# Performance work log

Hardware: AMD Instinct MI355X
Metric: run time of the kernel (lower is better)

The kernel has to match this reference:

```python
import jax, jax.numpy as jnp
import numpy as np

N, P = 65536, 1024

def setup_inputs() -> dict:
    key = jax.random.key(0)
    k1, k2, k3, k4 = jax.random.split(key, 4)
    X = jax.random.normal(k1, (N, P), dtype=jnp.float32)
    beta0 = jax.random.normal(k2, (1,), dtype=jnp.float32)
    beta = jax.random.normal(k3, (P,), dtype=jnp.float32)
    Theta = jax.random.normal(k4, (P, P), dtype=jnp.float32)
    return {"X": X, "beta0": beta0, "beta": beta, "Theta": Theta}

def reference(X, beta0, beta, Theta):
    # y_hat = beta0 + X @ beta + sum_{j<k} Theta[j,k] * X[:,j] * X[:,k]
    # The double loop uses only the strictly upper-triangular part of Theta.
    p = Theta.shape[0]
    theta_upper = jnp.triu(Theta, k=1)                     # [p, p]
    linear = beta0 + X @ beta                              # [n]
    interaction = jnp.sum((X @ theta_upper) * X, axis=1)   # [n], quadratic form
    return linear + interaction
```

## Files before the change

kernel.cpp:

```cpp
#include <hip/hip_runtime.h>


typedef __bf16 bf16_t;
typedef bf16_t bf16x8 __attribute__((ext_vector_type(8)));
typedef float f32x4 __attribute__((ext_vector_type(4)));
typedef unsigned short u16;
typedef u16 u16x4 __attribute__((ext_vector_type(4)));
typedef u16 u16x8 __attribute__((ext_vector_type(8)));

#define N_ROWS 65536
#define P_DIM  1024
#define BM 128
#define BN 128
#define BK 64

static __device__ __forceinline__ u16 f2bf(float f) {
  unsigned u = __builtin_bit_cast(unsigned, f);
  u += 0x7FFFu + ((u >> 16) & 1u);
  return (u16)(u >> 16);
}
static __device__ __forceinline__ float bf2f(u16 v) {
  return __builtin_bit_cast(float, ((unsigned)v) << 16);
}

static __device__ __forceinline__ void gload16(const void* g, void* lds_base) {
  __builtin_amdgcn_global_load_lds(
      (const __attribute__((address_space(1))) unsigned char*)g,
      (__attribute__((address_space(3))) unsigned char*)lds_base, 16, 0, 0);
}

__global__ void __launch_bounds__(256)
init_y(float* __restrict__ y, const float* __restrict__ beta0) {
  int i = blockIdx.x * blockDim.x + threadIdx.x;
  if (i < N_ROWS) y[i] = beta0[0];
}

__global__ void __launch_bounds__(256)
conv_x(const float* __restrict__ X, u16* __restrict__ Xb,
       float* __restrict__ y, const float* __restrict__ beta0) {
  const size_t tg = (size_t)blockIdx.x * 256 + threadIdx.x;
  if (tg < N_ROWS) y[tg] = beta0[0];
  const size_t nq = (size_t)N_ROWS * P_DIM / 8;
  const size_t stride = (size_t)gridDim.x * 256;
  for (size_t i = tg; i < nq; i += stride) {
    const int row = (int)(i >> 7);
    const int q   = (int)(i & 127);
    f32x4 a = *(const f32x4*)(X + i * 8);
    f32x4 b = *(const f32x4*)(X + i * 8 + 4);
    u16x8 w;
    #pragma unroll
    for (int j = 0; j < 4; ++j) { w[j] = f2bf(a[j]); w[j + 4] = f2bf(b[j]); }
    *(u16x8*)(Xb + (size_t)row * P_DIM + (size_t)((q ^ (row & 7)) * 8)) = w;
  }
}

__global__ void __launch_bounds__(128)
conv_theta(const float* __restrict__ Theta, u16* __restrict__ Tt) {
  __shared__ float tile[32][33];
  const int tid = threadIdx.x;
  const int k0  = blockIdx.x * 32;
  const int c0  = blockIdx.y * 32;
  {
    const int tx = tid & 31;
    const int rb = tid >> 5;
    #pragma unroll
    for (int i = 0; i < 8; ++i) {
      int kl = rb * 8 + i;
      tile[kl][tx] = Theta[(size_t)(k0 + kl) * P_DIM + c0 + tx];
    }
  }
  __syncthreads();
  {
    const int cl = tid >> 2;
    const int qt = tid & 3;
    const int c  = c0 + cl;
    const int Q  = blockIdx.x * 4 + qt;
    u16x8 w;
    #pragma unroll
    for (int e = 0; e < 8; ++e) {
      int k = Q * 8 + e;
      float v = tile[qt * 8 + e][cl];
      w[e] = (k < c) ? f2bf(v) : (u16)0;
    }
    *(u16x8*)(Tt + (size_t)c * P_DIM + (size_t)((Q ^ (c & 7)) * 8)) = w;
  }
}

__global__ void __launch_bounds__(512)
gemm_r12(const u16* __restrict__ Xb, const u16* __restrict__ Tt,
         const float* __restrict__ beta, float* __restrict__ y)
{
  __shared__ __align__(16) u16 L[2][16384];

  const int nwg = (N_ROWS / BM) * (P_DIM / BN);
  const int swz = (blockIdx.x & 7) * (nwg / 8) + (blockIdx.x >> 3);
  const int bn  = 7 - (swz & 7);
  const int bm  = swz >> 3;
  const int c0  = bn * BN;
  const int m0  = bm * BM;
  const int nkt = (bn + 1) * 2;

  const int tid  = threadIdx.x;
  const int lane = tid & 63;
  const int wid  = tid >> 6;
  const int wm   = wid >> 1;
  const int wn   = wid & 1;
  const int l15  = lane & 15;
  const int lg   = lane >> 4;

  const int srow = lane >> 3;
  const int sq   = (lane & 7) * 8;

  f32x4 acc[2][4];
  #pragma unroll
  for (int i = 0; i < 2; ++i)
    #pragma unroll
    for (int j = 0; j < 4; ++j)
      acc[i][j] = (f32x4)0.0f;

  #define STAGE(buf_, t_)                                                       \
    {                                                                           \
      const int kk_ = (t_) * BK;                                                \
      _Pragma("unroll")                                                         \
      for (int q = 0; q < 2; ++q) {                                             \
        const int ch_ = wid * 2 + q;                                            \
        gload16(Xb + (size_t)(m0 + ch_ * 8 + srow) * P_DIM + kk_ + sq,          \
                &L[buf_][ch_ * 512]);                                           \
        gload16(Tt + (size_t)(c0 + ch_ * 8 + srow) * P_DIM + kk_ + sq,          \
                &L[buf_][8192 + ch_ * 512]);                                    \
      }                                                                         \
    }

  STAGE(0, 0)
  asm volatile("s_waitcnt vmcnt(0)" ::: "memory");
  __builtin_amdgcn_sched_barrier(0);
  __builtin_amdgcn_s_barrier();
  __builtin_amdgcn_sched_barrier(0);

  for (int t = 0; t < nkt; ++t) {
    const int cur = t & 1;
    const bool pre = (t + 1 < nkt);
    if (pre) STAGE(cur ^ 1, t + 1)

    bf16x8 af[2][2], bfr[2][4];
    #pragma unroll
    for (int kk = 0; kk < 2; ++kk) {
      #pragma unroll
      for (int mi = 0; mi < 2; ++mi) {
        const int rw = wm * 32 + mi * 16 + l15;
        u16x8 v = *(const u16x8*)&L[cur][rw * 64 + ((kk * 4 + lg) ^ (rw & 7)) * 8];
        af[kk][mi] = __builtin_bit_cast(bf16x8, v);
      }
      #pragma unroll
      for (int ni = 0; ni < 4; ++ni) {
        const int cl = wn * 64 + ni * 16 + l15;
        u16x8 v = *(const u16x8*)&L[cur][8192 + cl * 64 + ((kk * 4 + lg) ^ (cl & 7)) * 8];
        bfr[kk][ni] = __builtin_bit_cast(bf16x8, v);
      }
    }

    __builtin_amdgcn_s_setprio(1);
    #pragma unroll
    for (int kk = 0; kk < 2; ++kk)
      #pragma unroll
      for (int mi = 0; mi < 2; ++mi)
        #pragma unroll
        for (int ni = 0; ni < 4; ++ni)
          acc[mi][ni] = __builtin_amdgcn_mfma_f32_16x16x32_bf16(bfr[kk][ni], af[kk][mi], acc[mi][ni], 0, 0, 0);
    __builtin_amdgcn_s_setprio(0);

    if (pre) { asm volatile("s_waitcnt vmcnt(0)" ::: "memory"); }
    __builtin_amdgcn_sched_barrier(0);
    __builtin_amdgcn_s_barrier();
    __builtin_amdgcn_sched_barrier(0);
  }
  #undef STAGE

  float ysum[2];
  ysum[0] = 0.0f; ysum[1] = 0.0f;

  #pragma unroll
  for (int mi = 0; mi < 2; ++mi) {
    const int row = m0 + wm * 32 + mi * 16 + l15;
    const size_t rbase = (size_t)row * P_DIM;
    const int rx = row & 7;
    #pragma unroll
    for (int ni = 0; ni < 4; ++ni) {
      const int cb = c0 + wn * 64 + ni * 16 + lg * 4;
      const int qx = cb >> 3;
      const int ex = cb & 7;
      u16x4 xw = *(const u16x4*)(Xb + rbase + ((size_t)((qx ^ rx) * 8) + ex));
      f32x4 bv = *(const f32x4*)(beta + cb);
      #pragma unroll
      for (int r = 0; r < 4; ++r)
        ysum[mi] += (acc[mi][ni][r] + bv[r]) * bf2f(xw[r]);
    }
  }

  #pragma unroll
  for (int mi = 0; mi < 2; ++mi) {
    ysum[mi] += __shfl_xor(ysum[mi], 16);
    ysum[mi] += __shfl_xor(ysum[mi], 32);
  }
  if (lane < 16) {
    #pragma unroll
    for (int mi = 0; mi < 2; ++mi)
      atomicAdd(&y[m0 + wm * 32 + mi * 16 + l15], ysum[mi]);
  }
}

#define LDT 40
__global__ void __launch_bounds__(256)
fused_quad_fallback(const float* __restrict__ X, const float* __restrict__ beta,
                    const float* __restrict__ Theta, float* __restrict__ y)
{
  __shared__ __align__(16) u16 Alds[128 * LDT];
  __shared__ __align__(16) u16 Blds[128 * LDT];

  const int bid = blockIdx.x;
  const int bn  = bid & 7;
  const int bm  = bid >> 3;
  const int c0  = bn * 128;
  const int m0  = bm * 128;
  const int nkt = (bn + 1) * 4;

  const int tid  = threadIdx.x;
  const int lane = tid & 63;
  const int wid  = tid >> 6;
  const int wm   = wid >> 1;
  const int wn   = wid & 1;
  const int l15  = lane & 15;
  const int lg   = lane >> 4;

  f32x4 acc[4][4];
  #pragma unroll
  for (int i = 0; i < 4; ++i)
    #pragma unroll
    for (int j = 0; j < 4; ++j)
      acc[i][j] = (f32x4)0.0f;

  const int arow  = tid >> 1;
  const int ahalf = (tid & 1) * 16;
  const int kb4 = (tid >> 5) * 4;
  const int cb4 = (tid & 31) * 4;

  for (int kt = 0; kt < nkt; ++kt) {
    const int k0 = kt * 32;
    __syncthreads();
    {
      const f32x4* p = (const f32x4*)(X + (size_t)(m0 + arow) * P_DIM + k0 + ahalf);
      f32x4 v0 = p[0], v1 = p[1], v2 = p[2], v3 = p[3];
      u16x8 w0, w1;
      #pragma unroll
      for (int i = 0; i < 4; ++i) {
        w0[i] = f2bf(v0[i]); w0[i + 4] = f2bf(v1[i]);
        w1[i] = f2bf(v2[i]); w1[i + 4] = f2bf(v3[i]);
      }
      *(u16x8*)&Alds[arow * LDT + ahalf]     = w0;
      *(u16x8*)&Alds[arow * LDT + ahalf + 8] = w1;
    }
    {
      float e[4][4];
      #pragma unroll
      for (int i = 0; i < 4; ++i) {
        f32x4 r = *(const f32x4*)(Theta + (size_t)(k0 + kb4 + i) * P_DIM + c0 + cb4);
        #pragma unroll
        for (int j = 0; j < 4; ++j)
          e[i][j] = ((k0 + kb4 + i) < (c0 + cb4 + j)) ? r[j] : 0.0f;
      }
      #pragma unroll
      for (int j = 0; j < 4; ++j) {
        u16x4 wv;
        #pragma unroll
        for (int i = 0; i < 4; ++i) wv[i] = f2bf(e[i][j]);
        *(u16x4*)&Blds[(cb4 + j) * LDT + kb4] = wv;
      }
    }
    __syncthreads();

    bf16x8 af[4], bfr[4];
    #pragma unroll
    for (int mi = 0; mi < 4; ++mi) {
      u16x8 t = *(const u16x8*)&Alds[(wm * 64 + mi * 16 + l15) * LDT + lg * 8];
      af[mi] = __builtin_bit_cast(bf16x8, t);
    }
    #pragma unroll
    for (int ni = 0; ni < 4; ++ni) {
      u16x8 t = *(const u16x8*)&Blds[(wn * 64 + ni * 16 + l15) * LDT + lg * 8];
      bfr[ni] = __builtin_bit_cast(bf16x8, t);
    }
    #pragma unroll
    for (int mi = 0; mi < 4; ++mi)
      #pragma unroll
      for (int ni = 0; ni < 4; ++ni)
        acc[mi][ni] = __builtin_amdgcn_mfma_f32_16x16x32_bf16(af[mi], bfr[ni], acc[mi][ni], 0, 0, 0);
  }

  float ysum[4][4];
  #pragma unroll
  for (int mi = 0; mi < 4; ++mi)
    #pragma unroll
    for (int r = 0; r < 4; ++r)
      ysum[mi][r] = 0.0f;

  #pragma unroll
  for (int ni = 0; ni < 4; ++ni) {
    const int col = c0 + wn * 64 + ni * 16 + l15;
    const float bta = beta[col];
    #pragma unroll
    for (int mi = 0; mi < 4; ++mi) {
      const int rowb = m0 + wm * 64 + mi * 16 + lg * 4;
      #pragma unroll
      for (int r = 0; r < 4; ++r) {
        float xv = X[(size_t)(rowb + r) * P_DIM + col];
        ysum[mi][r] += (acc[mi][ni][r] + bta) * xv;
      }
    }
  }

  #pragma unroll
  for (int m = 1; m < 16; m <<= 1)
    #pragma unroll
    for (int mi = 0; mi < 4; ++mi)
      #pragma unroll
      for (int r = 0; r < 4; ++r)
        ysum[mi][r] += __shfl_xor(ysum[mi][r], m);

  if (l15 == 0) {
    #pragma unroll
    for (int mi = 0; mi < 4; ++mi)
      #pragma unroll
      for (int r = 0; r < 4; ++r)
        atomicAdd(&y[m0 + wm * 64 + mi * 16 + lg * 4 + r], ysum[mi][r]);
  }
}

extern "C" void kernel_launch(void* const* d_in, const int* in_sizes, int n_in,
                              void* d_out, int out_size, void* d_ws, size_t ws_size,
                              hipStream_t stream) {
  const float* X     = (const float*)d_in[0];
  const float* beta0 = (const float*)d_in[1];
  const float* beta  = (const float*)d_in[2];
  const float* Theta = (const float*)d_in[3];
  float* y = (float*)d_out;

  const size_t need = (size_t)N_ROWS * P_DIM * 2 + (size_t)P_DIM * P_DIM * 2;
  if (ws_size >= need) {
    u16* Xb = (u16*)d_ws;
    u16* Tt = Xb + (size_t)N_ROWS * P_DIM;
    conv_x<<<2048, 256, 0, stream>>>(X, Xb, y, beta0);
    conv_theta<<<dim3(32, 32), 128, 0, stream>>>(Theta, Tt);
    gemm_r12<<<(N_ROWS / BM) * (P_DIM / BN), 512, 0, stream>>>(Xb, Tt, beta, y);
  } else {
    init_y<<<N_ROWS / 256, 256, 0, stream>>>(y, beta0);
    fused_quad_fallback<<<(N_ROWS / 128) * (P_DIM / 128), 256, 0, stream>>>(X, beta, Theta, y);
  }
}
```

Measured before the change: 180.0 us.

## Fuse X bf16 conversion into GEMM staging, drop separate conversion pass

Removes the standalone conv_x kernel, which read all of X in fp32 and wrote a bf16 copy. The GEMM now loads fp32 X tiles through registers, converts them to bf16 and writes them into swizzled LDS, and the epilogue reads fp32 X directly. BK is halved to 32 so the smaller LDS tiles fit, which doubles the number of k-iterations and barriers per tile. The y initialisation moves into conv_theta. The extra HBM round trip for X is gone, but X is now read in fp32 for every column tile, so GEMM-side traffic for X roughly doubles and staging now goes through registers.

```diff
diff --git a/kernel.cpp b/kernel.cpp
--- a/kernel.cpp
+++ b/kernel.cpp
@@ -12,16 +12,13 @@
 #define P_DIM  1024
 #define BM 128
 #define BN 128
-#define BK 64
+#define BK 32
 
 static __device__ __forceinline__ u16 f2bf(float f) {
   unsigned u = __builtin_bit_cast(unsigned, f);
   u += 0x7FFFu + ((u >> 16) & 1u);
   return (u16)(u >> 16);
 }
-static __device__ __forceinline__ float bf2f(u16 v) {
-  return __builtin_bit_cast(float, ((unsigned)v) << 16);
-}
 
 static __device__ __forceinline__ void gload16(const void* g, void* lds_base) {
   __builtin_amdgcn_global_load_lds(
@@ -35,29 +32,14 @@
   if (i < N_ROWS) y[i] = beta0[0];
 }
 
-__global__ void __launch_bounds__(256)
-conv_x(const float* __restrict__ X, u16* __restrict__ Xb,
-       float* __restrict__ y, const float* __restrict__ beta0) {
-  const size_t tg = (size_t)blockIdx.x * 256 + threadIdx.x;
-  if (tg < N_ROWS) y[tg] = beta0[0];
-  const size_t nq = (size_t)N_ROWS * P_DIM / 8;
-  const size_t stride = (size_t)gridDim.x * 256;
-  for (size_t i = tg; i < nq; i += stride) {
-    const int row = (int)(i >> 7);
-    const int q   = (int)(i & 127);
-    f32x4 a = *(const f32x4*)(X + i * 8);
-    f32x4 b = *(const f32x4*)(X + i * 8 + 4);
-    u16x8 w;
-    #pragma unroll
-    for (int j = 0; j < 4; ++j) { w[j] = f2bf(a[j]); w[j + 4] = f2bf(b[j]); }
-    *(u16x8*)(Xb + (size_t)row * P_DIM + (size_t)((q ^ (row & 7)) * 8)) = w;
-  }
-}
-
 __global__ void __launch_bounds__(128)
-conv_theta(const float* __restrict__ Theta, u16* __restrict__ Tt) {
+conv_theta(const float* __restrict__ Theta, u16* __restrict__ Tt,
+           float* __restrict__ y, const float* __restrict__ beta0) {
   __shared__ float tile[32][33];
   const int tid = threadIdx.x;
+  const int tg  = (blockIdx.y * gridDim.x + blockIdx.x) * 128 + tid;
+  if (tg < N_ROWS) y[tg] = beta0[0];
+
   const int k0  = blockIdx.x * 32;
   const int c0  = blockIdx.y * 32;
   {
@@ -82,15 +64,16 @@
       float v = tile[qt * 8 + e][cl];
       w[e] = (k < c) ? f2bf(v) : (u16)0;
     }
-    *(u16x8*)(Tt + (size_t)c * P_DIM + (size_t)((Q ^ (c & 7)) * 8)) = w;
+    const int qs = (qt ^ ((c >> 1) & 3));
+    *(u16x8*)(Tt + (size_t)c * P_DIM + (size_t)(blockIdx.x * 32 + qs * 8)) = w;
   }
 }
 
 __global__ void __launch_bounds__(512)
-gemm_r12(const u16* __restrict__ Xb, const u16* __restrict__ Tt,
+gemm_r13(const float* __restrict__ X, const u16* __restrict__ Tt,
          const float* __restrict__ beta, float* __restrict__ y)
 {
-  __shared__ __align__(16) u16 L[2][16384];
+  __shared__ __align__(16) u16 L[2][8192];
 
   const int nwg = (N_ROWS / BM) * (P_DIM / BN);
   const int swz = (blockIdx.x & 7) * (nwg / 8) + (blockIdx.x >> 3);
@@ -98,7 +81,7 @@
   const int bm  = swz >> 3;
   const int c0  = bn * BN;
   const int m0  = bm * BM;
-  const int nkt = (bn + 1) * 2;
+  const int nkt = (bn + 1) * 4;
 
   const int tid  = threadIdx.x;
   const int lane = tid & 63;
@@ -108,8 +91,12 @@
   const int l15  = lane & 15;
   const int lg   = lane >> 4;
 
-  const int srow = lane >> 3;
-  const int sq   = (lane & 7) * 8;
+  const int ar = tid >> 2;
+  const int ap = tid & 3;
+  const int aq = (ap ^ ((ar >> 1) & 3)) * 8;
+
+  const int brow = wid * 16 + (lane >> 2);
+  const int bq   = (lane & 3) * 8;
 
   f32x4 acc[2][4];
   #pragma unroll
@@ -118,21 +105,31 @@
     for (int j = 0; j < 4; ++j)
       acc[i][j] = (f32x4)0.0f;
 
-  #define STAGE(buf_, t_)                                                       \
+  f32x4 av0, av1;
+
+  #define STAGE_A_LOAD(t_)                                                      \
     {                                                                           \
-      const int kk_ = (t_) * BK;                                                \
+      const float* s_ = X + (size_t)(m0 + ar) * P_DIM + (t_) * BK + ap * 8;     \
+      av0 = ((const f32x4*)s_)[0];                                              \
+      av1 = ((const f32x4*)s_)[1];                                              \
+    }
+  #define STAGE_A_WRITE(buf_)                                                   \
+    {                                                                           \
+      u16x8 w_;                                                                 \
       _Pragma("unroll")                                                         \
-      for (int q = 0; q < 2; ++q) {                                             \
-        const int ch_ = wid * 2 + q;                                            \
-        gload16(Xb + (size_t)(m0 + ch_ * 8 + srow) * P_DIM + kk_ + sq,          \
-                &L[buf_][ch_ * 512]);                                           \
-        gload16(Tt + (size_t)(c0 + ch_ * 8 + srow) * P_DIM + kk_ + sq,          \
-                &L[buf_][8192 + ch_ * 512]);                                    \
-      }                                                                         \
-    }
-
-  STAGE(0, 0)
+      for (int j = 0; j < 4; ++j) { w_[j] = f2bf(av0[j]); w_[j + 4] = f2bf(av1[j]); } \
+      *(u16x8*)&L[buf_][ar * 32 + aq] = w_;                                     \
+    }
+  #define STAGE_B(buf_, t_)                                                     \
+    gload16(Tt + (size_t)(c0 + brow) * P_DIM + (t_) * BK + bq,                  \
+            &L[buf_][4096 + wid * 512]);
+
+  STAGE_A_LOAD(0)
+  STAGE_B(0, 0)
   asm volatile("s_waitcnt vmcnt(0)" ::: "memory");
+  __builtin_amdgcn_sched_barrier(0);
+  STAGE_A_WRITE(0)
+  asm volatile("s_waitcnt lgkmcnt(0)" ::: "memory");
   __builtin_amdgcn_sched_barrier(0);
   __builtin_amdgcn_s_barrier();
   __builtin_amdgcn_sched_barrier(0);
@@ -140,41 +137,43 @@
   for (int t = 0; t < nkt; ++t) {
     const int cur = t & 1;
     const bool pre = (t + 1 < nkt);
-    if (pre) STAGE(cur ^ 1, t + 1)
-
-    bf16x8 af[2][2], bfr[2][4];
-    #pragma unroll
-    for (int kk = 0; kk < 2; ++kk) {
-      #pragma unroll
-      for (int mi = 0; mi < 2; ++mi) {
-        const int rw = wm * 32 + mi * 16 + l15;
-        u16x8 v = *(const u16x8*)&L[cur][rw * 64 + ((kk * 4 + lg) ^ (rw & 7)) * 8];
-        af[kk][mi] = __builtin_bit_cast(bf16x8, v);
-      }
-      #pragma unroll
-      for (int ni = 0; ni < 4; ++ni) {
-        const int cl = wn * 64 + ni * 16 + l15;
-        u16x8 v = *(const u16x8*)&L[cur][8192 + cl * 64 + ((kk * 4 + lg) ^ (cl & 7)) * 8];
-        bfr[kk][ni] = __builtin_bit_cast(bf16x8, v);
-      }
+    if (pre) { STAGE_A_LOAD(t + 1) STAGE_B(cur ^ 1, t + 1) }
+
+    bf16x8 af[2], bfr[4];
+    #pragma unroll
+    for (int mi = 0; mi < 2; ++mi) {
+      const int rw = wm * 32 + mi * 16 + l15;
+      u16x8 v = *(const u16x8*)&L[cur][rw * 32 + (lg ^ ((rw >> 1) & 3)) * 8];
+      af[mi] = __builtin_bit_cast(bf16x8, v);
+    }
+    #pragma unroll
+    for (int ni = 0; ni < 4; ++ni) {
+      const int cl = wn * 64 + ni * 16 + l15;
+      u16x8 v = *(const u16x8*)&L[cur][4096 + cl * 32 + (lg ^ ((cl >> 1) & 3)) * 8];
+      bfr[ni] = __builtin_bit_cast(bf16x8, v);
     }
 
     __builtin_amdgcn_s_setprio(1);
     #pragma unroll
-    for (int kk = 0; kk < 2; ++kk)
-      #pragma unroll
-      for (int mi = 0; mi < 2; ++mi)
-        #pragma unroll
-        for (int ni = 0; ni < 4; ++ni)
-          acc[mi][ni] = __builtin_amdgcn_mfma_f32_16x16x32_bf16(bfr[kk][ni], af[kk][mi], acc[mi][ni], 0, 0, 0);
+    for (int mi = 0; mi < 2; ++mi)
+      #pragma unroll
+      for (int ni = 0; ni < 4; ++ni)
+        acc[mi][ni] = __builtin_amdgcn_mfma_f32_16x16x32_bf16(bfr[ni], af[mi], acc[mi][ni], 0, 0, 0);
     __builtin_amdgcn_s_setprio(0);
 
-    if (pre) { asm volatile("s_waitcnt vmcnt(0)" ::: "memory"); }
+    if (pre) {
+      asm volatile("s_waitcnt vmcnt(0)" ::: "memory");
+      __builtin_amdgcn_sched_barrier(0);
+      STAGE_A_WRITE(cur ^ 1)
+    }
+    asm volatile("s_waitcnt lgkmcnt(0)" ::: "memory");
     __builtin_amdgcn_sched_barrier(0);
     __builtin_amdgcn_s_barrier();
     __builtin_amdgcn_sched_barrier(0);
   }
-  #undef STAGE
+  #undef STAGE_A_LOAD
+  #undef STAGE_A_WRITE
+  #undef STAGE_B
 
   float ysum[2];
   ysum[0] = 0.0f; ysum[1] = 0.0f;
@@ -182,18 +181,15 @@
   #pragma unroll
   for (int mi = 0; mi < 2; ++mi) {
     const int row = m0 + wm * 32 + mi * 16 + l15;
-    const size_t rbase = (size_t)row * P_DIM;
-    const int rx = row & 7;
+    const float* xr = X + (size_t)row * P_DIM;
     #pragma unroll
     for (int ni = 0; ni < 4; ++ni) {
       const int cb = c0 + wn * 64 + ni * 16 + lg * 4;
-      const int qx = cb >> 3;
-      const int ex = cb & 7;
-      u16x4 xw = *(const u16x4*)(Xb + rbase + ((size_t)((qx ^ rx) * 8) + ex));
+      f32x4 xw = *(const f32x4*)(xr + cb);
       f32x4 bv = *(const f32x4*)(beta + cb);
       #pragma unroll
       for (int r = 0; r < 4; ++r)
-        ysum[mi] += (acc[mi][ni][r] + bv[r]) * bf2f(xw[r]);
+        ysum[mi] += (acc[mi][ni][r] + bv[r]) * xw[r];
     }
   }
 
@@ -344,13 +340,11 @@
   const float* Theta = (const float*)d_in[3];
   float* y = (float*)d_out;
 
-  const size_t need = (size_t)N_ROWS * P_DIM * 2 + (size_t)P_DIM * P_DIM * 2;
+  const size_t need = (size_t)P_DIM * P_DIM * 2;
   if (ws_size >= need) {
-    u16* Xb = (u16*)d_ws;
-    u16* Tt = Xb + (size_t)N_ROWS * P_DIM;
-    conv_x<<<2048, 256, 0, stream>>>(X, Xb, y, beta0);
-    conv_theta<<<dim3(32, 32), 128, 0, stream>>>(Theta, Tt);
-    gemm_r12<<<(N_ROWS / BM) * (P_DIM / BN), 512, 0, stream>>>(Xb, Tt, beta, y);
+    u16* Tt = (u16*)d_ws;
+    conv_theta<<<dim3(32, 32), 128, 0, stream>>>(Theta, Tt, y, beta0);
+    gemm_r13<<<(N_ROWS / BM) * (P_DIM / BN), 512, 0, stream>>>(X, Tt, beta, y);
   } else {
     init_y<<<N_ROWS / 256, 256, 0, stream>>>(y, beta0);
     fused_quad_fallback<<<(N_ROWS / 128) * (P_DIM / 128), 256, 0, stream>>>(X, beta, Theta, y);
```

New measurement: 163.6 us. 1.1x faster.
